# Performance work log

Measured on AMD Instinct MI355X. Metric: run time of the kernel, lower is better.

## Reference

```python
import jax, jax.numpy as jnp
import numpy as np

SEED_THR = 0.5
DUP_THR = 0.8


def _connected_labels(adj):
    """Min-label propagation with pointer jumping; adj: [N,N] bool (diag set for active nodes)."""
    N = adj.shape[0]

    def cond(carry):
        _, changed = carry
        return changed

    def body(carry):
        labels, _ = carry
        nbr_min = jnp.min(jnp.where(adj, labels[None, :], N), axis=1)
        new = jnp.minimum(labels, nbr_min)
        new = jnp.minimum(new, new[new])  # pointer jumping -> O(log N) convergence
        return new, jnp.any(new != labels)

    labels0 = jnp.arange(N)
    labels, _ = jax.lax.while_loop(cond, body, (labels0, jnp.array(True)))
    return labels


def _per_image(sig, scores):
    # sig: [N,C], scores: [N]
    N = sig.shape[0]
    idx = jnp.arange(N)
    sel = scores >= SEED_THR
    # fallback: if nothing passes the threshold, select argmax score
    sel = jnp.where(sel.any(), sel, idx == jnp.argmax(scores))

    # cosine pairwise similarity
    sn = sig * jax.lax.rsqrt(jnp.sum(sig * sig, axis=-1, keepdims=True) + 1e-12)
    sim = sn @ sn.T  # [N,N]

    adj = (sim >= DUP_THR) & sel[:, None] & sel[None, :]
    adj = adj | jnp.diag(sel)  # diagonal True for selected nodes

    labels = _connected_labels(adj)  # component root = min node index in component

    neg_inf = jnp.float32(-1e30)
    masked_scores = jnp.where(sel, scores, neg_inf)
    comp_max = jnp.full((N,), neg_inf, dtype=scores.dtype).at[labels].max(masked_scores)
    is_best = sel & (scores >= comp_max[labels])
    # tie-break: smallest index (matches torch argmax-first semantics)
    comp_best = jnp.full((N,), N, dtype=jnp.int32).at[labels].min(
        jnp.where(is_best, idx, N).astype(jnp.int32))
    is_seed = sel & (idx == comp_best[labels])

    # compact seeds to the front, ordered by component root (== DFS discovery order)
    sort_key = jnp.where(is_seed, labels, N)
    order = jnp.argsort(sort_key)
    mask = is_seed[order]  # [N] bool, True for valid seed slots
    seed_sig = jnp.where(mask[:, None], sig[order], jnp.zeros((), sig.dtype))
    seed_sc = jnp.where(mask, scores[order], jnp.zeros((), scores.dtype))
    return seed_sig, mask, seed_sc


def reference(query_signatures, query_seed_logits):
    L, B, Q, C = query_signatures.shape
    sig = jnp.transpose(query_signatures, (1, 0, 2, 3)).reshape(B, L * Q, C)
    logits = jnp.transpose(query_seed_logits, (1, 0, 2)).reshape(B, L * Q).astype(jnp.float32)
    scores = jax.nn.sigmoid(logits)
    seed_signatures, pad_mask, seed_scores = jax.vmap(_per_image)(sig, scores)
    return seed_signatures, pad_mask, seed_scores


def setup_inputs() -> dict:
    key = jax.random.key(0)
    k1, k2 = jax.random.split(key)
    L, B, Q, C = 6, 4, 900, 256
    return {
        "query_signatures": jax.random.normal(k1, (L, B, Q, C), dtype=jnp.float32),
        "query_seed_logits": jax.random.normal(k2, (L, B, Q), dtype=jnp.float32),
    }
```

## Files before the change

### kernel.cpp

```cpp
#include <hip/hip_runtime.h>
#include <cstdint>
#include <cstddef>

#define LDIM 6
#define BDIM 4
#define QDIM 900
#define CDIM 256
#define NDIM (LDIM*QDIM)
#define NN   5408
#define TT   85
#define NTRI (TT*(TT+1)/2)

typedef short bf16x8 __attribute__((ext_vector_type(8)));
typedef float floatx4 __attribute__((ext_vector_type(4)));

__device__ __forceinline__ int sig_off(int b, int n) {
    int l = n / QDIM, q = n - l * QDIM;
    return ((l * BDIM + b) * QDIM + q) * CDIM;
}
__device__ __forceinline__ int logit_off(int b, int n) {
    int l = n / QDIM, q = n - l * QDIM;
    return (l * BDIM + b) * QDIM + q;
}

__device__ __forceinline__ int uf_load(const int* p, int i) {
    return __hip_atomic_load(&p[i], __ATOMIC_RELAXED, __HIP_MEMORY_SCOPE_AGENT);
}
__device__ int uf_find(int* p, int x) {
    int r = x;
    int pr = uf_load(p, r);
    while (pr != r) { r = pr; pr = uf_load(p, r); }
    return r;
}
__device__ void uf_union(int* p, int a, int b) {
    int ra = uf_find(p, a), rb = uf_find(p, b);
    while (ra != rb) {
        int hi = ra > rb ? ra : rb;
        int lo = ra ^ rb ^ hi;
        int old = atomicCAS(&p[hi], hi, lo);
        if (old == hi) return;
        ra = uf_find(p, old);
        rb = uf_find(p, lo);
    }
}

__device__ __forceinline__ unsigned short f2bf(float f) {
    unsigned int u = __float_as_uint(f);
    u += 0x7fffu + ((u >> 16) & 1u);
    return (unsigned short)(u >> 16);
}

__global__ __launch_bounds__(1024) void k_prep(const float* __restrict__ logits,
                                               float* __restrict__ scores,
                                               int* __restrict__ parent,
                                               int* __restrict__ selIdx,
                                               int* __restrict__ Mcnt) {
    int b = blockIdx.x, t = threadIdx.x;
    int lane = t & 63, w = t >> 6;
    __shared__ int wsum[16];
    __shared__ unsigned long long wkey[16];
    __shared__ int sbase;
    if (t == 0) sbase = 0;
    unsigned long long mykey = 0ULL;
    __syncthreads();
    for (int base = 0; base < NDIM; base += 1024) {
        int n = base + t;
        int f = 0;
        if (n < NDIM) {
            float x = logits[logit_off(b, n)];
            float sc = 1.0f / (1.0f + expf(-x));
            scores[b * NN + n] = sc;
            parent[b * NN + n] = n;
            f = (sc >= 0.5f) ? 1 : 0;
            unsigned long long key =
                ((unsigned long long)__float_as_uint(sc) << 32) | (unsigned int)(~n);
            if (key > mykey) mykey = key;
        }
        unsigned long long bal = __ballot(f != 0);
        int rank = __popcll(bal & ((1ull << lane) - 1ull));
        if (lane == 0) wsum[w] = __popcll(bal);
        __syncthreads();
        if (t == 0) {
            int s = sbase;
            for (int i = 0; i < 16; i++) { int v = wsum[i]; wsum[i] = s; s += v; }
            sbase = s;
        }
        __syncthreads();
        if (f) selIdx[b * NN + wsum[w] + rank] = n;
        __syncthreads();
    }
    for (int off = 32; off; off >>= 1) {
        unsigned long long o = __shfl_down(mykey, off);
        if (o > mykey) mykey = o;
    }
    if (lane == 0) wkey[w] = mykey;
    __syncthreads();
    if (t == 0) {
        if (sbase == 0) {
            unsigned long long k = 0ULL;
            for (int i = 0; i < 16; i++) if (wkey[i] > k) k = wkey[i];
            selIdx[b * NN + 0] = (int)(~(unsigned int)(k & 0xffffffffULL));
            Mcnt[b] = 1;
        } else {
            Mcnt[b] = sbase;
        }
    }
}

__global__ void k_tobf(const float* __restrict__ sig, const int* __restrict__ selIdx,
                       const int* __restrict__ Mcnt, unsigned short* __restrict__ Xbf) {
    int b = blockIdx.y;
    int g = (blockIdx.x * blockDim.x + threadIdx.x) >> 6;
    int lane = threadIdx.x & 63;
    if (g >= Mcnt[b]) return;
    int node = selIdx[b * NN + g];
    const float4 v = *(const float4*)(sig + sig_off(b, node) + lane * 4);
    float s = v.x * v.x + v.y * v.y + v.z * v.z + v.w * v.w;
    for (int off = 32; off; off >>= 1) s += __shfl_down(s, off);
    s = __shfl(s, 0);
    float ninv = rsqrtf(s + 1e-12f);
    ushort4 o;
    o.x = f2bf(v.x * ninv); o.y = f2bf(v.y * ninv);
    o.z = f2bf(v.z * ninv); o.w = f2bf(v.w * ninv);
    int c = lane >> 1;
    int sc = c ^ (g & 7);
    *(ushort4*)(Xbf + ((size_t)(b * NN + g)) * CDIM + sc * 8 + (lane & 1) * 4) = o;
}

__global__ __launch_bounds__(256) void k_sim_mfma(const unsigned short* __restrict__ Xbf,
                                                  const int* __restrict__ selIdx,
                                                  const int* __restrict__ Mcnt,
                                                  int* __restrict__ parent) {
    int bx = blockIdx.x;
    int b = bx & 3;
    int t = bx >> 2;
    int M = Mcnt[b];
    int ti = (int)((sqrtf(8.0f * (float)t + 1.0f) - 1.0f) * 0.5f);
    while ((ti + 1) * (ti + 2) / 2 <= t) ti++;
    while (ti * (ti + 1) / 2 > t) ti--;
    int tj = t - ti * (ti + 1) / 2;
    if (ti * 64 >= M) return;

    __shared__ char Bs[32768];

    int tid = threadIdx.x;
    int lane = tid & 63, wave = tid >> 6;
    int rsel = lane & 15, quad = lane >> 4;

    const char* xb = (const char*)Xbf + ((size_t)b * NN) * 512;
#pragma unroll
    for (int k = 0; k < 8; k++) {
        int i = wave * 8 + k;
        int row = min(tj * 64 + 2 * i, NN - 2);
        const char* src = xb + (size_t)row * 512 + lane * 16;
        __builtin_amdgcn_global_load_lds(
            (const __attribute__((address_space(1))) unsigned int*)src,
            (__attribute__((address_space(3))) unsigned int*)(Bs + i * 1024),
            16, 0, 0);
    }

    int gA = min(ti * 64 + wave * 16 + rsel, M - 1);
    const unsigned short* pA = Xbf + ((size_t)(b * NN + gA)) * CDIM;
    int swA = gA & 7;
    int swB = rsel & 7;

    __syncthreads();

    floatx4 acc[4] = {{0.f,0.f,0.f,0.f},{0.f,0.f,0.f,0.f},{0.f,0.f,0.f,0.f},{0.f,0.f,0.f,0.f}};
#pragma unroll
    for (int ks = 0; ks < CDIM / 32; ks++) {
        bf16x8 a = *(const bf16x8*)(pA + (((ks * 4 + quad) ^ swA) << 3));
#pragma unroll
        for (int nj = 0; nj < 4; nj++) {
            const char* pb = Bs + (nj * 16 + rsel) * 512 + (((ks * 4 + quad) ^ swB) << 4);
            bf16x8 bb = *(const bf16x8*)pb;
            acc[nj] = __builtin_amdgcn_mfma_f32_16x16x32_bf16(a, bb, acc[nj], 0, 0, 0);
        }
    }

    int rowA = ti * 64 + wave * 16 + quad * 4;
#pragma unroll
    for (int nj = 0; nj < 4; nj++) {
        int gj = tj * 64 + nj * 16 + rsel;
#pragma unroll
        for (int r = 0; r < 4; r++) {
            int gi = rowA + r;
            if (gi < M && gj < M && gi > gj && acc[nj][r] >= 0.8f) {
                uf_union(parent + b * NN, selIdx[b * NN + gi], selIdx[b * NN + gj]);
            }
        }
    }
}

__global__ __launch_bounds__(1024) void k_comp(int* __restrict__ parent,
                                               const int* __restrict__ selIdx,
                                               const int* __restrict__ Mcnt,
                                               const float* __restrict__ scores,
                                               unsigned long long* __restrict__ compKey,
                                               int* __restrict__ seedNode,
                                               int* __restrict__ Scnt) {
    int b = blockIdx.x, t = threadIdx.x;
    int lane = t & 63, w = t >> 6;
    __shared__ int wsum[16];
    __shared__ int sbase;

    for (int n = t; n < NN; n += 1024) compKey[b * NN + n] = 0ULL;
    if (t == 0) sbase = 0;
    __syncthreads();

    int M = Mcnt[b];
    for (int base = 0; base < M; base += 1024) {
        int g = base + t;
        if (g < M) {
            int node = selIdx[b * NN + g];
            int root = uf_find(parent + b * NN, node);
            unsigned long long key =
                ((unsigned long long)__float_as_uint(scores[b * NN + node]) << 32) |
                (unsigned int)(~node);
            atomicMax(&compKey[b * NN + root], key);
        }
    }
    __syncthreads();

    for (int base = 0; base < NDIM; base += 1024) {
        int n = base + t;
        unsigned long long key = 0ULL;
        if (n < NDIM)
            key = __hip_atomic_load(&compKey[b * NN + n], __ATOMIC_RELAXED,
                                    __HIP_MEMORY_SCOPE_AGENT);
        int f = (key != 0ULL) ? 1 : 0;
        unsigned long long bal = __ballot(f != 0);
        int rank = __popcll(bal & ((1ull << lane) - 1ull));
        if (lane == 0) wsum[w] = __popcll(bal);
        __syncthreads();
        if (t == 0) {
            int s = sbase;
            for (int i = 0; i < 16; i++) { int v = wsum[i]; wsum[i] = s; s += v; }
            sbase = s;
        }
        __syncthreads();
        if (f) seedNode[b * NN + wsum[w] + rank] = (int)(~(unsigned int)(key & 0xffffffffULL));
        __syncthreads();
    }
    if (t == 0) Scnt[b] = sbase;
}

__global__ void k_write(const float* __restrict__ sig, const float* __restrict__ scores,
                        const int* __restrict__ seedNode, const int* __restrict__ Scnt,
                        float* __restrict__ out) {
    int b = blockIdx.y;
    int slot = blockIdx.x * 4 + (threadIdx.x >> 6);
    int lane = threadIdx.x & 63;
    float* orow = out + ((size_t)(b * NDIM + slot)) * CDIM + lane * 4;
    if (slot < Scnt[b]) {
        int s = seedNode[b * NN + slot];
        float4 v = *(const float4*)(sig + sig_off(b, s) + lane * 4);
        *(float4*)orow = v;
        if (lane == 0) {
            out[(size_t)BDIM * NDIM * CDIM + (size_t)b * NDIM + slot] = 1.0f;
            out[(size_t)BDIM * NDIM * CDIM + (size_t)BDIM * NDIM + (size_t)b * NDIM + slot] =
                scores[b * NN + s];
        }
    } else {
        float4 z = {0.f, 0.f, 0.f, 0.f};
        *(float4*)orow = z;
        if (lane == 0) {
            out[(size_t)BDIM * NDIM * CDIM + (size_t)b * NDIM + slot] = 0.0f;
            out[(size_t)BDIM * NDIM * CDIM + (size_t)BDIM * NDIM + (size_t)b * NDIM + slot] = 0.0f;
        }
    }
}

extern "C" void kernel_launch(void* const* d_in, const int* in_sizes, int n_in,
                              void* d_out, int out_size, void* d_ws, size_t ws_size,
                              hipStream_t stream) {
    (void)in_sizes; (void)n_in; (void)out_size; (void)ws_size;
    const float* sig = (const float*)d_in[0];
    const float* logits = (const float*)d_in[1];
    float* out = (float*)d_out;
    char* ws = (char*)d_ws;

    const size_t arr = (size_t)BDIM * NN * 4;
    int* Mcnt = (int*)(ws + 0);
    int* Scnt = (int*)(ws + 64);
    unsigned long long* compKey = (unsigned long long*)(ws + 256);
    float* scores = (float*)(ws + 256 + 2 * arr);
    int* parent   = (int*)(ws + 256 + 3 * arr);
    int* selIdx   = (int*)(ws + 256 + 4 * arr);
    int* seedNode = (int*)(ws + 256 + 5 * arr);
    unsigned short* Xbf = (unsigned short*)(ws + 256 + 6 * arr);

    k_prep<<<BDIM, 1024, 0, stream>>>(logits, scores, parent, selIdx, Mcnt);
    k_tobf<<<dim3((NDIM + 3) / 4, BDIM), 256, 0, stream>>>(sig, selIdx, Mcnt, Xbf);
    k_sim_mfma<<<NTRI * BDIM, 256, 0, stream>>>(Xbf, selIdx, Mcnt, parent);
    k_comp<<<BDIM, 1024, 0, stream>>>(parent, selIdx, Mcnt, scores, compKey, seedNode, Scnt);
    k_write<<<dim3(NDIM / 4, BDIM), 256, 0, stream>>>(sig, scores, seedNode, Scnt, out);
}
```

Baseline: 115.7 us.

## Enlarge similarity tiles to 128x128 with two A fragments per wave

```diff
diff --git a/kernel.cpp b/kernel.cpp
--- a/kernel.cpp
+++ b/kernel.cpp
@@ -8,8 +8,8 @@
 #define CDIM 256
 #define NDIM (LDIM*QDIM)
 #define NN   5408
-#define TT   85
-#define NTRI (TT*(TT+1)/2)
+#define T128 43
+#define NT128 (T128*(T128+1)/2)
 
 typedef short bf16x8 __attribute__((ext_vector_type(8)));
 typedef float floatx4 __attribute__((ext_vector_type(4)));
@@ -139,9 +139,9 @@
     while ((ti + 1) * (ti + 2) / 2 <= t) ti++;
     while (ti * (ti + 1) / 2 > t) ti--;
     int tj = t - ti * (ti + 1) / 2;
-    if (ti * 64 >= M) return;
-
-    __shared__ char Bs[32768];
+    if (ti * 128 >= M) return;
+
+    extern __shared__ char Bs[];
 
     int tid = threadIdx.x;
     int lane = tid & 63, wave = tid >> 6;
@@ -149,9 +149,9 @@
 
     const char* xb = (const char*)Xbf + ((size_t)b * NN) * 512;
 #pragma unroll
-    for (int k = 0; k < 8; k++) {
-        int i = wave * 8 + k;
-        int row = min(tj * 64 + 2 * i, NN - 2);
+    for (int k = 0; k < 16; k++) {
+        int i = wave * 16 + k;
+        int row = min(tj * 128 + 2 * i, NN - 2);
         const char* src = xb + (size_t)row * 512 + lane * 16;
         __builtin_amdgcn_global_load_lds(
             (const __attribute__((address_space(1))) unsigned int*)src,
@@ -159,34 +159,48 @@
             16, 0, 0);
     }
 
-    int gA = min(ti * 64 + wave * 16 + rsel, M - 1);
-    const unsigned short* pA = Xbf + ((size_t)(b * NN + gA)) * CDIM;
-    int swA = gA & 7;
+    int rA = ti * 128 + wave * 32;
+    int gA0 = min(rA + rsel, M - 1);
+    int gA1 = min(rA + 16 + rsel, M - 1);
+    const char* pA0 = (const char*)Xbf + ((size_t)(b * NN + gA0)) * 512;
+    const char* pA1 = (const char*)Xbf + ((size_t)(b * NN + gA1)) * 512;
+    int swA0 = gA0 & 7, swA1 = gA1 & 7;
     int swB = rsel & 7;
 
     __syncthreads();
 
-    floatx4 acc[4] = {{0.f,0.f,0.f,0.f},{0.f,0.f,0.f,0.f},{0.f,0.f,0.f,0.f},{0.f,0.f,0.f,0.f}};
+    floatx4 acc[2][8];
+#pragma unroll
+    for (int s = 0; s < 2; s++)
+#pragma unroll
+        for (int nj = 0; nj < 8; nj++) acc[s][nj] = (floatx4){0.f, 0.f, 0.f, 0.f};
+
 #pragma unroll
     for (int ks = 0; ks < CDIM / 32; ks++) {
-        bf16x8 a = *(const bf16x8*)(pA + (((ks * 4 + quad) ^ swA) << 3));
-#pragma unroll
-        for (int nj = 0; nj < 4; nj++) {
-            const char* pb = Bs + (nj * 16 + rsel) * 512 + (((ks * 4 + quad) ^ swB) << 4);
-            bf16x8 bb = *(const bf16x8*)pb;
-            acc[nj] = __builtin_amdgcn_mfma_f32_16x16x32_bf16(a, bb, acc[nj], 0, 0, 0);
-        }
-    }
-
-    int rowA = ti * 64 + wave * 16 + quad * 4;
-#pragma unroll
-    for (int nj = 0; nj < 4; nj++) {
-        int gj = tj * 64 + nj * 16 + rsel;
-#pragma unroll
-        for (int r = 0; r < 4; r++) {
-            int gi = rowA + r;
-            if (gi < M && gj < M && gi > gj && acc[nj][r] >= 0.8f) {
-                uf_union(parent + b * NN, selIdx[b * NN + gi], selIdx[b * NN + gj]);
+        int cq = ks * 4 + quad;
+        bf16x8 a0 = *(const bf16x8*)(pA0 + ((cq ^ swA0) << 4));
+        bf16x8 a1 = *(const bf16x8*)(pA1 + ((cq ^ swA1) << 4));
+        int cb = (cq ^ swB) << 4;
+#pragma unroll
+        for (int nj = 0; nj < 8; nj++) {
+            bf16x8 bb = *(const bf16x8*)(Bs + (nj * 16 + rsel) * 512 + cb);
+            acc[0][nj] = __builtin_amdgcn_mfma_f32_16x16x32_bf16(a0, bb, acc[0][nj], 0, 0, 0);
+            acc[1][nj] = __builtin_amdgcn_mfma_f32_16x16x32_bf16(a1, bb, acc[1][nj], 0, 0, 0);
+        }
+    }
+
+#pragma unroll
+    for (int s = 0; s < 2; s++) {
+        int rowA = rA + s * 16 + quad * 4;
+#pragma unroll
+        for (int nj = 0; nj < 8; nj++) {
+            int gj = tj * 128 + nj * 16 + rsel;
+#pragma unroll
+            for (int r = 0; r < 4; r++) {
+                int gi = rowA + r;
+                if (gi < M && gj < M && gi > gj && acc[s][nj][r] >= 0.8f) {
+                    uf_union(parent + b * NN, selIdx[b * NN + gi], selIdx[b * NN + gj]);
+                }
             }
         }
     }
@@ -292,7 +306,7 @@
 
     k_prep<<<BDIM, 1024, 0, stream>>>(logits, scores, parent, selIdx, Mcnt);
     k_tobf<<<dim3((NDIM + 3) / 4, BDIM), 256, 0, stream>>>(sig, selIdx, Mcnt, Xbf);
-    k_sim_mfma<<<NTRI * BDIM, 256, 0, stream>>>(Xbf, selIdx, Mcnt, parent);
+    k_sim_mfma<<<NT128 * BDIM, 256, 65536, stream>>>(Xbf, selIdx, Mcnt, parent);
     k_comp<<<BDIM, 1024, 0, stream>>>(parent, selIdx, Mcnt, scores, compKey, seedNode, Scnt);
     k_write<<<dim3(NDIM / 4, BDIM), 256, 0, stream>>>(sig, scores, seedNode, Scnt, out);
 }
```

Measured after the change: 112.5 us. -2.7%, faster.
